# Performance work log

Hardware: AMD Instinct MI355X
Metric: run time of the kernel (lower is better)

## Reference

```python
import jax, jax.numpy as jnp
import numpy as np

HIDDEN = 128
N_RBF = 20
K = 16
CUTOFF = 5.0


def setup_inputs() -> dict:
    key = jax.random.key(0)
    ks = jax.random.split(key, 12)
    B, N, D = 8, 4096, HIDDEN
    edge_in = 2 * D + N_RBF  # 276
    s = 0.02
    return {
        "h": jax.random.normal(ks[0], (B, N, D), jnp.float32),
        "positions": jax.random.normal(ks[1], (B, N, 3), jnp.float32),
        # edge MLP: Linear(276->128), SiLU, Linear(128->128), SiLU
        "ew1": jax.random.normal(ks[2], (edge_in, D), jnp.float32) * s,
        "eb1": jnp.zeros((D,), jnp.float32),
        "ew2": jax.random.normal(ks[3], (D, D), jnp.float32) * s,
        "eb2": jnp.zeros((D,), jnp.float32),
        # node MLP: Linear(256->128), SiLU, (Dropout=identity in eval), Linear(128->128)
        "nw1": jax.random.normal(ks[4], (2 * D, D), jnp.float32) * s,
        "nb1": jnp.zeros((D,), jnp.float32),
        "nw2": jax.random.normal(ks[5], (D, D), jnp.float32) * s,
        "nb2": jnp.zeros((D,), jnp.float32),
        # LayerNorm
        "gamma": jnp.ones((D,), jnp.float32),
        "beta": jnp.zeros((D,), jnp.float32),
    }


def reference(h, positions, ew1, eb1, ew2, eb2, nw1, nb1, nw2, nb2, gamma, beta):
    B, N, D = h.shape
    k = min(K, N - 1)

    # ---- kNN graph build (dense pairwise, self masked with +inf) ----
    diff = positions[:, :, None, :] - positions[:, None, :, :]      # [B,N,N,3]
    dists = jnp.sqrt(jnp.sum(diff * diff, axis=-1) + 1e-8)          # [B,N,N]
    eye = jnp.eye(N, dtype=bool)
    dists_masked = jnp.where(eye[None], jnp.inf, dists)
    _, edge_idx = jax.lax.top_k(-dists_masked, k)                   # [B,N,k] smallest dists
    edge_dist = jnp.take_along_axis(dists_masked, edge_idx, axis=-1)  # [B,N,k]
    edge_mask = edge_dist < CUTOFF                                  # [B,N,k]

    # ---- RBF distance encoding (non-trainable buffers) ----
    centers = jnp.linspace(0.0, CUTOFF, N_RBF)                      # [n_rbf]
    widths = (CUTOFF / N_RBF) ** (-2)
    rbf = jnp.exp(-widths * (edge_dist[..., None] - centers) ** 2)  # [B,N,k,n_rbf]

    # ---- gather neighbor features ----
    h_j = jax.vmap(lambda hb, ib: hb[ib])(h, edge_idx)              # [B,N,k,D]
    h_i = jnp.broadcast_to(h[:, :, None, :], h_j.shape)             # [B,N,k,D]
    edge_features = jnp.concatenate([h_i, h_j, rbf], axis=-1)       # [B,N,k,2D+n_rbf]

    # ---- edge MLP + mask + scatter-sum aggregate ----
    m = jax.nn.silu(edge_features @ ew1 + eb1)
    m = jax.nn.silu(m @ ew2 + eb2)
    m = m * edge_mask[..., None].astype(m.dtype)
    agg = jnp.sum(m, axis=2)                                        # [B,N,D]

    # ---- node MLP (dropout is identity at eval) + residual + LayerNorm ----
    node_in = jnp.concatenate([h, agg], axis=-1)                    # [B,N,2D]
    update = jax.nn.silu(node_in @ nw1 + nb1) @ nw2 + nb2
    x = h + update
    mu = jnp.mean(x, axis=-1, keepdims=True)
    var = jnp.mean((x - mu) ** 2, axis=-1, keepdims=True)
    return (x - mu) / jnp.sqrt(var + 1e-5) * gamma + beta
```

## Files before the change

### kernel.cpp

```cpp
#include <hip/hip_runtime.h>

#define HID 128
#define NRBF 20
#define KNN 16
#define NNODE 4096
#define NBATCH 8
#define CAP 112

typedef __attribute__((ext_vector_type(8))) short short8;
typedef __attribute__((ext_vector_type(4))) float f32x4;

__device__ __forceinline__ short f2bf(float x) {
  unsigned u = __builtin_bit_cast(unsigned, x);
  u = u + 0x7FFFu + ((u >> 16) & 1u);
  return (short)(u >> 16);
}
__device__ __forceinline__ float silu_f(float x) {
  return x * __builtin_amdgcn_rcpf(1.0f + __expf(-x));
}
__device__ __forceinline__ short8 cv8(const float* p) {
  f32x4 a = *(const f32x4*)p;
  f32x4 b = *(const f32x4*)(p + 4);
  short8 r;
  r[0]=f2bf(a[0]); r[1]=f2bf(a[1]); r[2]=f2bf(a[2]); r[3]=f2bf(a[3]);
  r[4]=f2bf(b[0]); r[5]=f2bf(b[1]); r[6]=f2bf(b[2]); r[7]=f2bf(b[3]);
  return r;
}

__global__ __launch_bounds__(256)
void hcvt_kernel(const float* __restrict__ h, short* __restrict__ hb)
{
  size_t i = ((size_t)blockIdx.x * 256 + threadIdx.x) * 8;
  *(short8*)(hb + i) = cv8(h + i);
}

__global__ __launch_bounds__(512)
void knn_kernel(const float* __restrict__ pos,
                int* __restrict__ eidx, float* __restrict__ edist)
{
  __shared__ float pX[NNODE], pY[NNODE], pZ[NNODE];
  __shared__ float d2b[8][4][CAP];
  __shared__ int   jb[8][4][CAP];
  __shared__ int   cntL[8][4];

  const int tid  = threadIdx.x;
  const int wv   = tid >> 6;
  const int lane = tid & 63;
  const int b    = blockIdx.x >> 7;
  const int grp  = blockIdx.x & 127;

  const float* pb = pos + (size_t)b * NNODE * 3;
  for (int idx = tid; idx < NNODE; idx += 512) {
    pX[idx] = pb[idx*3]; pY[idx] = pb[idx*3+1]; pZ[idx] = pb[idx*3+2];
  }
  __syncthreads();

  const int i0 = grp * 32 + wv * 4;
  float pix[4], piy[4], piz[4];
  #pragma unroll
  for (int n = 0; n < 4; ++n) { pix[n]=pX[i0+n]; piy[n]=pY[i0+n]; piz[n]=pZ[i0+n]; }

  float vmin[4] = {3.0e38f, 3.0e38f, 3.0e38f, 3.0e38f};
  #pragma unroll 4
  for (int t = 0; t < 64; ++t) {
    const int j = t * 64 + lane;
    const float x = pX[j], y = pY[j], z = pZ[j];
    #pragma unroll
    for (int n = 0; n < 4; ++n) {
      float dx = pix[n] - x, dy = piy[n] - y, dz = piz[n] - z;
      float d2 = fmaf(dz, dz, fmaf(dy, dy, dx * dx));
      vmin[n] = fminf(vmin[n], d2);
    }
  }

  float Tp[4];
  #pragma unroll
  for (int n = 0; n < 4; ++n) {
    float v = vmin[n];
    #pragma unroll
    for (int k = 2; k <= 64; k <<= 1) {
      #pragma unroll
      for (int jj = k >> 1; jj > 0; jj >>= 1) {
        float o = __shfl_xor(v, jj);
        const bool up   = ((lane & k) == 0);
        const bool lowl = ((lane & jj) == 0);
        float mn = fminf(v, o), mx = fmaxf(v, o);
        v = (up == lowl) ? mn : mx;
      }
    }
    float Tf = __shfl(v, 16);
    Tp[n] = Tf * (1.0f + 2.0e-6f) + 1.0e-35f;
  }

  if (lane < 4) cntL[wv][lane] = 0;
  #pragma unroll 2
  for (int t = 0; t < 64; ++t) {
    const int j = t * 64 + lane;
    const float x = pX[j], y = pY[j], z = pZ[j];
    #pragma unroll
    for (int n = 0; n < 4; ++n) {
      float dx = pix[n] - x, dy = piy[n] - y, dz = piz[n] - z;
      float d2 = fmaf(dz, dz, fmaf(dy, dy, dx * dx));
      if ((j != i0 + n) && (d2 <= Tp[n])) {
        int p = atomicAdd(&cntL[wv][n], 1);
        if (p < CAP) jb[wv][n][p] = j;
      }
    }
  }

  #pragma unroll 1
  for (int n = 0; n < 4; ++n) {
    int cnt = cntL[wv][n];
    if (cnt > CAP) cnt = CAP;
    for (int s = lane; s < cnt; s += 64) {
      int j = jb[wv][n][s];
      float dx = __fsub_rn(pix[n], pX[j]);
      float dy = __fsub_rn(piy[n], pY[j]);
      float dz = __fsub_rn(piz[n], pZ[j]);
      d2b[wv][n][s] = __fadd_rn(__fadd_rn(__fmul_rn(dx,dx), __fmul_rn(dy,dy)),
                                __fmul_rn(dz,dz));
    }
    for (int s = lane; s < cnt; s += 64) {
      float dm = d2b[wv][n][s]; int jm = jb[wv][n][s];
      int rank = 0;
      for (int c = 0; c < cnt; ++c) {
        float dc = d2b[wv][n][c]; int jc = jb[wv][n][c];
        if (dc < dm || (dc == dm && jc < jm)) ++rank;
      }
      if (rank < KNN) {
        size_t base = ((size_t)b * NNODE + i0 + n) * KNN;
        eidx[base + rank]  = b * NNODE + jm;
        edist[base + rank] = sqrtf(__fadd_rn(dm, 1e-8f));
      }
    }
  }
}

#define ENPW 16

template<bool HBF>
__global__ __launch_bounds__(512)
void edge_kernel(const float* __restrict__ h, const short* __restrict__ hb,
                 const int* __restrict__ eidx, const float* __restrict__ edist,
                 const float* __restrict__ ew1, const float* __restrict__ eb1,
                 const float* __restrict__ ew2, const float* __restrict__ eb2,
                 float* __restrict__ agg)
{
  __shared__ __attribute__((aligned(16))) short8 F1[9*8*64];
  __shared__ __attribute__((aligned(16))) short8 F2[4*8*64];
  __shared__ __attribute__((aligned(16))) short m1s[8][2048];

  const int tid = threadIdx.x;
  for (int f = tid; f < 9*8*64; f += 512) {
    int kc = f >> 9, rem = f & 511, nf = rem >> 6, ln = rem & 63;
    int kb = kc*32 + (ln >> 4)*8, col = nf*16 + (ln & 15);
    short8 v;
    #pragma unroll
    for (int e = 0; e < 8; ++e) {
      int k = kb + e;
      v[e] = (k < 276) ? f2bf(ew1[k*128 + col]) : (short)0;
    }
    F1[f] = v;
  }
  for (int f = tid; f < 4*8*64; f += 512) {
    int kc = f >> 9, rem = f & 511, nf = rem >> 6, ln = rem & 63;
    int kb = kc*32 + (ln >> 4)*8, col = nf*16 + (ln & 15);
    short8 v;
    #pragma unroll
    for (int e = 0; e < 8; ++e) v[e] = f2bf(ew2[(kb + e)*128 + col]);
    F2[f] = v;
  }
  __syncthreads();

  const int wv = tid >> 6, lane = tid & 63;
  const int lo = lane & 15, hi = lane >> 4;
  short* m1w = &m1s[wv][0];

  float b1v[8], b2v[8];
  #pragma unroll
  for (int nf = 0; nf < 8; ++nf) {
    b1v[nf] = eb1[nf*16 + lo];
    b2v[nf] = eb2[nf*16 + lo];
  }
  int wbase[4], xmask[4], rbase[4];
  #pragma unroll
  for (int q = 0; q < 4; ++q) {
    int row = hi*4 + q;
    wbase[q] = (row << 8) + (lo << 1);
    xmask[q] = (row & 7) << 4;
  }
  #pragma unroll
  for (int kc = 0; kc < 4; ++kc)
    rbase[kc] = ((lo << 8) + ((kc*32 + hi*8) << 1)) ^ ((lo & 7) << 4);

  const f32x4 zero4 = {0.f, 0.f, 0.f, 0.f};
  const int nbase = (blockIdx.x * 8 + wv) * ENPW;

  #pragma unroll 1
  for (int it = 0; it < ENPW/2; ++it) {
    const int nA = nbase + it*2, nB = nA + 1;
    int jgA = eidx[(size_t)nA*KNN + lo] & (NBATCH*NNODE - 1);
    int jgB = eidx[(size_t)nB*KNN + lo] & (NBATCH*NNODE - 1);
    const float deA = edist[(size_t)nA*KNN + lo];
    const float deB = edist[(size_t)nB*KNN + lo];

    short8 aIA[4], aJA[4], aIB[4], aJB[4];
    #pragma unroll
    for (int kc = 0; kc < 4; ++kc) {
      if constexpr (HBF) {
        aIA[kc] = *(const short8*)(hb + (size_t)nA*HID  + kc*32 + hi*8);
        aJA[kc] = *(const short8*)(hb + (size_t)jgA*HID + kc*32 + hi*8);
        aIB[kc] = *(const short8*)(hb + (size_t)nB*HID  + kc*32 + hi*8);
        aJB[kc] = *(const short8*)(hb + (size_t)jgB*HID + kc*32 + hi*8);
      } else {
        aIA[kc] = cv8(h + (size_t)nA*HID  + kc*32 + hi*8);
        aJA[kc] = cv8(h + (size_t)jgA*HID + kc*32 + hi*8);
        aIB[kc] = cv8(h + (size_t)nB*HID  + kc*32 + hi*8);
        aJB[kc] = cv8(h + (size_t)jgB*HID + kc*32 + hi*8);
      }
    }
    short8 aRA, aRB;
    #pragma unroll
    for (int e = 0; e < 8; ++e) {
      const int r = hi*8 + e;
      float vA = 0.f, vB = 0.f;
      if (r < NRBF) {
        const float cr = (float)(r * (5.0/19.0));
        float tA = __fsub_rn(deA, cr), tB = __fsub_rn(deB, cr);
        vA = __expf(-16.0f * __fmul_rn(tA, tA));
        vB = __expf(-16.0f * __fmul_rn(tB, tB));
      }
      aRA[e] = f2bf(vA); aRB[e] = f2bf(vB);
    }

    f32x4 acc1A[8], acc1B[8];
    #pragma unroll
    for (int nf = 0; nf < 8; ++nf) { acc1A[nf] = zero4; acc1B[nf] = zero4; }
    __builtin_amdgcn_s_setprio(1);
    #pragma unroll
    for (int kc = 0; kc < 9; ++kc) {
      short8 aA = (kc < 4) ? aIA[kc] : ((kc < 8) ? aJA[kc-4] : aRA);
      short8 aB = (kc < 4) ? aIB[kc] : ((kc < 8) ? aJB[kc-4] : aRB);
      #pragma unroll
      for (int nf = 0; nf < 8; ++nf) {
        short8 bf = F1[(kc*8 + nf)*64 + lane];
        acc1A[nf] = __builtin_amdgcn_mfma_f32_16x16x32_bf16(aA, bf, acc1A[nf], 0,0,0);
        acc1B[nf] = __builtin_amdgcn_mfma_f32_16x16x32_bf16(aB, bf, acc1B[nf], 0,0,0);
      }
    }
    __builtin_amdgcn_s_setprio(0);

    short8 a2A[4], a2B[4];
    #pragma unroll
    for (int nf = 0; nf < 8; ++nf) {
      #pragma unroll
      for (int q = 0; q < 4; ++q) {
        int off = (wbase[q] + (nf << 5)) ^ xmask[q];
        *(short*)((char*)m1w + off) = f2bf(silu_f(acc1A[nf][q] + b1v[nf]));
      }
    }
    #pragma unroll
    for (int kc = 0; kc < 4; ++kc)
      a2A[kc] = *(const short8*)((char*)m1w + rbase[kc]);
    #pragma unroll
    for (int nf = 0; nf < 8; ++nf) {
      #pragma unroll
      for (int q = 0; q < 4; ++q) {
        int off = (wbase[q] + (nf << 5)) ^ xmask[q];
        *(short*)((char*)m1w + off) = f2bf(silu_f(acc1B[nf][q] + b1v[nf]));
      }
    }
    #pragma unroll
    for (int kc = 0; kc < 4; ++kc)
      a2B[kc] = *(const short8*)((char*)m1w + rbase[kc]);

    f32x4 acc2A[8], acc2B[8];
    #pragma unroll
    for (int nf = 0; nf < 8; ++nf) { acc2A[nf] = zero4; acc2B[nf] = zero4; }
    __builtin_amdgcn_s_setprio(1);
    #pragma unroll
    for (int kc = 0; kc < 4; ++kc) {
      #pragma unroll
      for (int nf = 0; nf < 8; ++nf) {
        short8 bf = F2[(kc*8 + nf)*64 + lane];
        acc2A[nf] = __builtin_amdgcn_mfma_f32_16x16x32_bf16(a2A[kc], bf, acc2A[nf], 0,0,0);
        acc2B[nf] = __builtin_amdgcn_mfma_f32_16x16x32_bf16(a2B[kc], bf, acc2B[nf], 0,0,0);
      }
    }
    __builtin_amdgcn_s_setprio(0);

    float dqA[4], dqB[4];
    #pragma unroll
    for (int q = 0; q < 4; ++q) {
      dqA[q] = __shfl(deA, hi*4 + q);
      dqB[q] = __shfl(deB, hi*4 + q);
    }
    #pragma unroll
    for (int nf = 0; nf < 8; ++nf) {
      float sA = 0.f, sB = 0.f;
      #pragma unroll
      for (int q = 0; q < 4; ++q) {
        float mA = silu_f(acc2A[nf][q] + b2v[nf]);
        float mB = silu_f(acc2B[nf][q] + b2v[nf]);
        sA += (dqA[q] < 5.0f) ? mA : 0.f;
        sB += (dqB[q] < 5.0f) ? mB : 0.f;
      }
      sA += __shfl_xor(sA, 16); sA += __shfl_xor(sA, 32);
      sB += __shfl_xor(sB, 16); sB += __shfl_xor(sB, 32);
      if (hi == 0) {
        agg[(size_t)nA*HID + nf*16 + lo] = sA;
        agg[(size_t)nB*HID + nf*16 + lo] = sB;
      }
    }
  }
}

template<bool HBF>
__global__ __launch_bounds__(512)
void node_kernel(const float* __restrict__ h, const short* __restrict__ hb,
                 const float* agg,
                 const float* __restrict__ nw1, const float* __restrict__ nb1,
                 const float* __restrict__ nw2, const float* __restrict__ nb2,
                 const float* __restrict__ gam, const float* __restrict__ bet,
                 float* out)
{
  __shared__ __attribute__((aligned(16))) short8 G1[8*8*64];
  __shared__ __attribute__((aligned(16))) short8 G2[4*8*64];
  __shared__ __attribute__((aligned(16))) short m1s[8][2048];

  const int tid = threadIdx.x;
  for (int f = tid; f < 8*8*64; f += 512) {
    int kc = f >> 9, rem = f & 511, nf = rem >> 6, ln = rem & 63;
    int kb = kc*32 + (ln >> 4)*8, col = nf*16 + (ln & 15);
    short8 v;
    #pragma unroll
    for (int e = 0; e < 8; ++e) v[e] = f2bf(nw1[(kb + e)*128 + col]);
    G1[f] = v;
  }
  for (int f = tid; f < 4*8*64; f += 512) {
    int kc = f >> 9, rem = f & 511, nf = rem >> 6, ln = rem & 63;
    int kb = kc*32 + (ln >> 4)*8, col = nf*16 + (ln & 15);
    short8 v;
    #pragma unroll
    for (int e = 0; e < 8; ++e) v[e] = f2bf(nw2[(kb + e)*128 + col]);
    G2[f] = v;
  }
  __syncthreads();

  const int wv = tid >> 6, lane = tid & 63;
  const int lo = lane & 15, hi = lane >> 4;
  short* m1w = &m1s[wv][0];

  float b1v[8], b2v[8], gv[8], bv[8];
  #pragma unroll
  for (int nf = 0; nf < 8; ++nf) {
    b1v[nf] = nb1[nf*16 + lo];
    b2v[nf] = nb2[nf*16 + lo];
    gv[nf]  = gam[nf*16 + lo];
    bv[nf]  = bet[nf*16 + lo];
  }
  const f32x4 zero4 = {0.f, 0.f, 0.f, 0.f};

  const int row0 = (blockIdx.x * 8 + wv) * 16;

  const float* hrow = h   + (size_t)(row0 + lo) * HID;
  const float* arow = agg + (size_t)(row0 + lo) * HID;
  const short* hbrow = hb + (size_t)(row0 + lo) * HID;

  f32x4 acc1[8];
  #pragma unroll
  for (int nf = 0; nf < 8; ++nf) acc1[nf] = zero4;
  #pragma unroll
  for (int kc = 0; kc < 8; ++kc) {
    short8 a;
    if (kc < 4) {
      if constexpr (HBF) a = *(const short8*)(hbrow + kc*32 + hi*8);
      else               a = cv8(hrow + kc*32 + hi*8);
    } else {
      a = cv8(arow + (kc - 4)*32 + hi*8);
    }
    #pragma unroll
    for (int nf = 0; nf < 8; ++nf) {
      short8 bf = G1[(kc*8 + nf)*64 + lane];
      acc1[nf] = __builtin_amdgcn_mfma_f32_16x16x32_bf16(a, bf, acc1[nf], 0,0,0);
    }
  }

  #pragma unroll
  for (int nf = 0; nf < 8; ++nf) {
    #pragma unroll
    for (int q = 0; q < 4; ++q) {
      float s = silu_f(acc1[nf][q] + b1v[nf]);
      int row = hi*4 + q, col = nf*16 + lo;
      int byteoff = ((row << 8) + (col << 1)) ^ ((row & 7) << 4);
      *(short*)((char*)m1w + byteoff) = f2bf(s);
    }
  }

  f32x4 acc2[8];
  #pragma unroll
  for (int nf = 0; nf < 8; ++nf) acc2[nf] = zero4;
  #pragma unroll
  for (int kc = 0; kc < 4; ++kc) {
    int byteA = ((lo << 8) + ((kc*32 + hi*8) << 1)) ^ ((lo & 7) << 4);
    short8 a = *(const short8*)((char*)m1w + byteA);
    #pragma unroll
    for (int nf = 0; nf < 8; ++nf) {
      short8 bf = G2[(kc*8 + nf)*64 + lane];
      acc2[nf] = __builtin_amdgcn_mfma_f32_16x16x32_bf16(a, bf, acc2[nf], 0,0,0);
    }
  }

  float xv[4][8];
  #pragma unroll
  for (int nf = 0; nf < 8; ++nf) {
    #pragma unroll
    for (int q = 0; q < 4; ++q) {
      xv[q][nf] = acc2[nf][q] + b2v[nf]
                + h[(size_t)(row0 + hi*4 + q) * HID + nf*16 + lo];
    }
  }

  #pragma unroll
  for (int q = 0; q < 4; ++q) {
    float s = 0.0f;
    #pragma unroll
    for (int nf = 0; nf < 8; ++nf) s += xv[q][nf];
    s += __shfl_xor(s, 1); s += __shfl_xor(s, 2);
    s += __shfl_xor(s, 4); s += __shfl_xor(s, 8);
    float mu = s * 0.0078125f;
    float t = 0.0f;
    #pragma unroll
    for (int nf = 0; nf < 8; ++nf) { float d = xv[q][nf] - mu; t += d * d; }
    t += __shfl_xor(t, 1); t += __shfl_xor(t, 2);
    t += __shfl_xor(t, 4); t += __shfl_xor(t, 8);
    float inv = 1.0f / sqrtf(t * 0.0078125f + 1e-5f);
    #pragma unroll
    for (int nf = 0; nf < 8; ++nf) {
      float y = (xv[q][nf] - mu) * inv * gv[nf] + bv[nf];
      out[(size_t)(row0 + hi*4 + q) * HID + nf*16 + lo] = y;
    }
  }
}

extern "C" void kernel_launch(void* const* d_in, const int* in_sizes, int n_in,
                              void* d_out, int out_size, void* d_ws, size_t ws_size,
                              hipStream_t stream) {
  (void)in_sizes; (void)n_in; (void)out_size;
  const float* h   = (const float*)d_in[0];
  const float* pos = (const float*)d_in[1];
  const float* ew1 = (const float*)d_in[2];
  const float* eb1 = (const float*)d_in[3];
  const float* ew2 = (const float*)d_in[4];
  const float* eb2 = (const float*)d_in[5];
  const float* nw1 = (const float*)d_in[6];
  const float* nb1 = (const float*)d_in[7];
  const float* nw2 = (const float*)d_in[8];
  const float* nb2 = (const float*)d_in[9];
  const float* gam = (const float*)d_in[10];
  const float* bet = (const float*)d_in[11];

  const size_t base_need = (size_t)NBATCH * NNODE * KNN * 8;
  const size_t hbf_need  = base_need + (size_t)NBATCH * NNODE * HID * 2;
  if (ws_size < base_need) return;
  const bool use_hbf = (ws_size >= hbf_need);

  char* wsp = (char*)d_ws;
  int*   eidx  = (int*)wsp;
  float* edist = (float*)(wsp + (size_t)NBATCH * NNODE * KNN * 4);
  short* hb    = (short*)(wsp + base_need);
  float* agg   = (float*)d_out;

  if (use_hbf) {
    hcvt_kernel<<<dim3(2048), dim3(256), 0, stream>>>(h, hb);
  }
  knn_kernel<<<dim3(1024), dim3(512), 0, stream>>>(pos, eidx, edist);
  if (use_hbf) {
    edge_kernel<true ><<<dim3(256), dim3(512), 0, stream>>>(h, hb, eidx, edist,
                                                            ew1, eb1, ew2, eb2, agg);
    node_kernel<true ><<<dim3(256), dim3(512), 0, stream>>>(h, hb, agg, nw1, nb1,
                                                            nw2, nb2, gam, bet, (float*)d_out);
  } else {
    edge_kernel<false><<<dim3(256), dim3(512), 0, stream>>>(h, hb, eidx, edist,
                                                            ew1, eb1, ew2, eb2, agg);
    node_kernel<false><<<dim3(256), dim3(512), 0, stream>>>(h, hb, agg, nw1, nb1,
                                                            nw2, nb2, gam, bet, (float*)d_out);
  }
}
```

Measured before the change: 203.5 us.

## Double-buffer edge-kernel gathers and split kNN min reduction into two chains

The edge kernel now software-pipelines its work: the neighbour and self feature gathers for the next pair of nodes are issued into a second register set while the current pair runs its MFMA chain, so global-load latency is meant to hide behind compute. The kNN threshold scan also processes two candidate columns per iteration with separate min accumulators, which shortens the dependency chain. In exchange, register pressure in the edge kernel roughly doubles for the A-operand fragments. That raises the risk of spills or lower occupancy at 512 threads per block.

```diff
diff --git a/kernel.cpp b/kernel.cpp
--- a/kernel.cpp
+++ b/kernel.cpp
@@ -60,23 +60,26 @@
   #pragma unroll
   for (int n = 0; n < 4; ++n) { pix[n]=pX[i0+n]; piy[n]=pY[i0+n]; piz[n]=pZ[i0+n]; }
 
-  float vmin[4] = {3.0e38f, 3.0e38f, 3.0e38f, 3.0e38f};
+  float vmin0[4] = {3.0e38f, 3.0e38f, 3.0e38f, 3.0e38f};
+  float vmin1[4] = {3.0e38f, 3.0e38f, 3.0e38f, 3.0e38f};
   #pragma unroll 4
-  for (int t = 0; t < 64; ++t) {
-    const int j = t * 64 + lane;
-    const float x = pX[j], y = pY[j], z = pZ[j];
+  for (int t = 0; t < 64; t += 2) {
+    const int j0 = t*64 + lane, j1 = j0 + 64;
+    const float x0 = pX[j0], y0 = pY[j0], z0 = pZ[j0];
+    const float x1 = pX[j1], y1 = pY[j1], z1 = pZ[j1];
     #pragma unroll
     for (int n = 0; n < 4; ++n) {
-      float dx = pix[n] - x, dy = piy[n] - y, dz = piz[n] - z;
-      float d2 = fmaf(dz, dz, fmaf(dy, dy, dx * dx));
-      vmin[n] = fminf(vmin[n], d2);
+      float dx0 = pix[n]-x0, dy0 = piy[n]-y0, dz0 = piz[n]-z0;
+      vmin0[n] = fminf(vmin0[n], fmaf(dz0,dz0, fmaf(dy0,dy0, dx0*dx0)));
+      float dx1 = pix[n]-x1, dy1 = piy[n]-y1, dz1 = piz[n]-z1;
+      vmin1[n] = fminf(vmin1[n], fmaf(dz1,dz1, fmaf(dy1,dy1, dx1*dx1)));
     }
   }
 
   float Tp[4];
   #pragma unroll
   for (int n = 0; n < 4; ++n) {
-    float v = vmin[n];
+    float v = fminf(vmin0[n], vmin1[n]);
     #pragma unroll
     for (int k = 2; k <= 64; k <<= 1) {
       #pragma unroll
@@ -139,6 +142,128 @@
 #define ENPW 16
 
 template<bool HBF>
+__device__ __forceinline__ void load_pair(const float* __restrict__ h,
+                 const short* __restrict__ hb,
+                 const int* __restrict__ eidx, const float* __restrict__ edist,
+                 int nA, int nB, int lo, int hi,
+                 short8 (&aIA)[4], short8 (&aJA)[4],
+                 short8 (&aIB)[4], short8 (&aJB)[4],
+                 float& deA, float& deB)
+{
+  int jgA = eidx[(size_t)nA*KNN + lo] & (NBATCH*NNODE - 1);
+  int jgB = eidx[(size_t)nB*KNN + lo] & (NBATCH*NNODE - 1);
+  deA = edist[(size_t)nA*KNN + lo];
+  deB = edist[(size_t)nB*KNN + lo];
+  #pragma unroll
+  for (int kc = 0; kc < 4; ++kc) {
+    if constexpr (HBF) {
+      aIA[kc] = *(const short8*)(hb + (size_t)nA*HID  + kc*32 + hi*8);
+      aJA[kc] = *(const short8*)(hb + (size_t)jgA*HID + kc*32 + hi*8);
+      aIB[kc] = *(const short8*)(hb + (size_t)nB*HID  + kc*32 + hi*8);
+      aJB[kc] = *(const short8*)(hb + (size_t)jgB*HID + kc*32 + hi*8);
+    } else {
+      aIA[kc] = cv8(h + (size_t)nA*HID  + kc*32 + hi*8);
+      aJA[kc] = cv8(h + (size_t)jgA*HID + kc*32 + hi*8);
+      aIB[kc] = cv8(h + (size_t)nB*HID  + kc*32 + hi*8);
+      aJB[kc] = cv8(h + (size_t)jgB*HID + kc*32 + hi*8);
+    }
+  }
+}
+
+#define COMPUTE_PAIR(AIA, AJA, AIB, AJB, DEA, DEB, NA, NB)                      \
+  do {                                                                          \
+    short8 aRA, aRB;                                                            \
+    _Pragma("unroll")                                                           \
+    for (int e = 0; e < 8; ++e) {                                               \
+      const int r = hi*8 + e;                                                   \
+      float vA = 0.f, vB = 0.f;                                                 \
+      if (r < NRBF) {                                                           \
+        const float cr = (float)(r * (5.0/19.0));                               \
+        float tA = __fsub_rn(DEA, cr), tB = __fsub_rn(DEB, cr);                 \
+        vA = __expf(-16.0f * __fmul_rn(tA, tA));                                \
+        vB = __expf(-16.0f * __fmul_rn(tB, tB));                                \
+      }                                                                         \
+      aRA[e] = f2bf(vA); aRB[e] = f2bf(vB);                                     \
+    }                                                                           \
+    f32x4 acc1A[8], acc1B[8];                                                   \
+    _Pragma("unroll")                                                           \
+    for (int nf = 0; nf < 8; ++nf) { acc1A[nf] = zero4; acc1B[nf] = zero4; }    \
+    __builtin_amdgcn_s_setprio(1);                                              \
+    _Pragma("unroll")                                                           \
+    for (int kc = 0; kc < 9; ++kc) {                                            \
+      short8 aA = (kc < 4) ? AIA[kc] : ((kc < 8) ? AJA[kc-4] : aRA);            \
+      short8 aB = (kc < 4) ? AIB[kc] : ((kc < 8) ? AJB[kc-4] : aRB);            \
+      _Pragma("unroll")                                                         \
+      for (int nf = 0; nf < 8; ++nf) {                                          \
+        short8 bfv = F1[(kc*8 + nf)*64 + lane];                                 \
+        acc1A[nf] = __builtin_amdgcn_mfma_f32_16x16x32_bf16(aA, bfv, acc1A[nf], 0,0,0); \
+        acc1B[nf] = __builtin_amdgcn_mfma_f32_16x16x32_bf16(aB, bfv, acc1B[nf], 0,0,0); \
+      }                                                                         \
+    }                                                                           \
+    __builtin_amdgcn_s_setprio(0);                                              \
+    short8 a2A[4], a2B[4];                                                      \
+    _Pragma("unroll")                                                           \
+    for (int nf = 0; nf < 8; ++nf) {                                            \
+      _Pragma("unroll")                                                         \
+      for (int q = 0; q < 4; ++q) {                                             \
+        int off = (wbase[q] + (nf << 5)) ^ xmask[q];                            \
+        *(short*)((char*)m1w + off) = f2bf(silu_f(acc1A[nf][q] + b1v[nf]));     \
+      }                                                                         \
+    }                                                                           \
+    _Pragma("unroll")                                                           \
+    for (int kc = 0; kc < 4; ++kc)                                              \
+      a2A[kc] = *(const short8*)((char*)m1w + rbase[kc]);                       \
+    _Pragma("unroll")                                                           \
+    for (int nf = 0; nf < 8; ++nf) {                                            \
+      _Pragma("unroll")                                                         \
+      for (int q = 0; q < 4; ++q) {                                             \
+        int off = (wbase[q] + (nf << 5)) ^ xmask[q];                            \
+        *(short*)((char*)m1w + off) = f2bf(silu_f(acc1B[nf][q] + b1v[nf]));     \
+      }                                                                         \
+    }                                                                           \
+    _Pragma("unroll")                                                           \
+    for (int kc = 0; kc < 4; ++kc)                                              \
+      a2B[kc] = *(const short8*)((char*)m1w + rbase[kc]);                       \
+    f32x4 acc2A[8], acc2B[8];                                                   \
+    _Pragma("unroll")                                                           \
+    for (int nf = 0; nf < 8; ++nf) { acc2A[nf] = zero4; acc2B[nf] = zero4; }    \
+    __builtin_amdgcn_s_setprio(1);                                              \
+    _Pragma("unroll")                                                           \
+    for (int kc = 0; kc < 4; ++kc) {                                            \
+      _Pragma("unroll")                                                         \
+      for (int nf = 0; nf < 8; ++nf) {                                          \
+        short8 bfv = F2[(kc*8 + nf)*64 + lane];                                 \
+        acc2A[nf] = __builtin_amdgcn_mfma_f32_16x16x32_bf16(a2A[kc], bfv, acc2A[nf], 0,0,0); \
+        acc2B[nf] = __builtin_amdgcn_mfma_f32_16x16x32_bf16(a2B[kc], bfv, acc2B[nf], 0,0,0); \
+      }                                                                         \
+    }                                                                           \
+    __builtin_amdgcn_s_setprio(0);                                              \
+    float dqA[4], dqB[4];                                                       \
+    _Pragma("unroll")                                                           \
+    for (int q = 0; q < 4; ++q) {                                               \
+      dqA[q] = __shfl(DEA, hi*4 + q);                                           \
+      dqB[q] = __shfl(DEB, hi*4 + q);                                           \
+    }                                                                           \
+    _Pragma("unroll")                                                           \
+    for (int nf = 0; nf < 8; ++nf) {                                            \
+      float sA = 0.f, sB = 0.f;                                                 \
+      _Pragma("unroll")                                                         \
+      for (int q = 0; q < 4; ++q) {                                             \
+        float mA = silu_f(acc2A[nf][q] + b2v[nf]);                              \
+        float mB = silu_f(acc2B[nf][q] + b2v[nf]);                              \
+        sA += (dqA[q] < 5.0f) ? mA : 0.f;                                       \
+        sB += (dqB[q] < 5.0f) ? mB : 0.f;                                       \
+      }                                                                         \
+      sA += __shfl_xor(sA, 16); sA += __shfl_xor(sA, 32);                       \
+      sB += __shfl_xor(sB, 16); sB += __shfl_xor(sB, 32);                       \
+      if (hi == 0) {                                                            \
+        agg[(size_t)(NA)*HID + nf*16 + lo] = sA;                                \
+        agg[(size_t)(NB)*HID + nf*16 + lo] = sB;                                \
+      }                                                                         \
+    }                                                                           \
+  } while (0)
+
+template<bool HBF>
 __global__ __launch_bounds__(512)
 void edge_kernel(const float* __restrict__ h, const short* __restrict__ hb,
                  const int* __restrict__ eidx, const float* __restrict__ edist,
@@ -196,122 +321,22 @@
   const f32x4 zero4 = {0.f, 0.f, 0.f, 0.f};
   const int nbase = (blockIdx.x * 8 + wv) * ENPW;
 
+  short8 p0IA[4], p0JA[4], p0IB[4], p0JB[4]; float p0dA, p0dB;
+  short8 p1IA[4], p1JA[4], p1IB[4], p1JB[4]; float p1dA, p1dB;
+
+  load_pair<HBF>(h, hb, eidx, edist, nbase+0, nbase+1, lo, hi,
+                 p0IA, p0JA, p0IB, p0JB, p0dA, p0dB);
+
   #pragma unroll 1
-  for (int it = 0; it < ENPW/2; ++it) {
-    const int nA = nbase + it*2, nB = nA + 1;
-    int jgA = eidx[(size_t)nA*KNN + lo] & (NBATCH*NNODE - 1);
-    int jgB = eidx[(size_t)nB*KNN + lo] & (NBATCH*NNODE - 1);
-    const float deA = edist[(size_t)nA*KNN + lo];
-    const float deB = edist[(size_t)nB*KNN + lo];
-
-    short8 aIA[4], aJA[4], aIB[4], aJB[4];
-    #pragma unroll
-    for (int kc = 0; kc < 4; ++kc) {
-      if constexpr (HBF) {
-        aIA[kc] = *(const short8*)(hb + (size_t)nA*HID  + kc*32 + hi*8);
-        aJA[kc] = *(const short8*)(hb + (size_t)jgA*HID + kc*32 + hi*8);
-        aIB[kc] = *(const short8*)(hb + (size_t)nB*HID  + kc*32 + hi*8);
-        aJB[kc] = *(const short8*)(hb + (size_t)jgB*HID + kc*32 + hi*8);
-      } else {
-        aIA[kc] = cv8(h + (size_t)nA*HID  + kc*32 + hi*8);
-        aJA[kc] = cv8(h + (size_t)jgA*HID + kc*32 + hi*8);
-        aIB[kc] = cv8(h + (size_t)nB*HID  + kc*32 + hi*8);
-        aJB[kc] = cv8(h + (size_t)jgB*HID + kc*32 + hi*8);
-      }
-    }
-    short8 aRA, aRB;
-    #pragma unroll
-    for (int e = 0; e < 8; ++e) {
-      const int r = hi*8 + e;
-      float vA = 0.f, vB = 0.f;
-      if (r < NRBF) {
-        const float cr = (float)(r * (5.0/19.0));
-        float tA = __fsub_rn(deA, cr), tB = __fsub_rn(deB, cr);
-        vA = __expf(-16.0f * __fmul_rn(tA, tA));
-        vB = __expf(-16.0f * __fmul_rn(tB, tB));
-      }
-      aRA[e] = f2bf(vA); aRB[e] = f2bf(vB);
-    }
-
-    f32x4 acc1A[8], acc1B[8];
-    #pragma unroll
-    for (int nf = 0; nf < 8; ++nf) { acc1A[nf] = zero4; acc1B[nf] = zero4; }
-    __builtin_amdgcn_s_setprio(1);
-    #pragma unroll
-    for (int kc = 0; kc < 9; ++kc) {
-      short8 aA = (kc < 4) ? aIA[kc] : ((kc < 8) ? aJA[kc-4] : aRA);
-      short8 aB = (kc < 4) ? aIB[kc] : ((kc < 8) ? aJB[kc-4] : aRB);
-      #pragma unroll
-      for (int nf = 0; nf < 8; ++nf) {
-        short8 bf = F1[(kc*8 + nf)*64 + lane];
-        acc1A[nf] = __builtin_amdgcn_mfma_f32_16x16x32_bf16(aA, bf, acc1A[nf], 0,0,0);
-        acc1B[nf] = __builtin_amdgcn_mfma_f32_16x16x32_bf16(aB, bf, acc1B[nf], 0,0,0);
-      }
-    }
-    __builtin_amdgcn_s_setprio(0);
-
-    short8 a2A[4], a2B[4];
-    #pragma unroll
-    for (int nf = 0; nf < 8; ++nf) {
-      #pragma unroll
-      for (int q = 0; q < 4; ++q) {
-        int off = (wbase[q] + (nf << 5)) ^ xmask[q];
-        *(short*)((char*)m1w + off) = f2bf(silu_f(acc1A[nf][q] + b1v[nf]));
-      }
-    }
-    #pragma unroll
-    for (int kc = 0; kc < 4; ++kc)
-      a2A[kc] = *(const short8*)((char*)m1w + rbase[kc]);
-    #pragma unroll
-    for (int nf = 0; nf < 8; ++nf) {
-      #pragma unroll
-      for (int q = 0; q < 4; ++q) {
-        int off = (wbase[q] + (nf << 5)) ^ xmask[q];
-        *(short*)((char*)m1w + off) = f2bf(silu_f(acc1B[nf][q] + b1v[nf]));
-      }
-    }
-    #pragma unroll
-    for (int kc = 0; kc < 4; ++kc)
-      a2B[kc] = *(const short8*)((char*)m1w + rbase[kc]);
-
-    f32x4 acc2A[8], acc2B[8];
-    #pragma unroll
-    for (int nf = 0; nf < 8; ++nf) { acc2A[nf] = zero4; acc2B[nf] = zero4; }
-    __builtin_amdgcn_s_setprio(1);
-    #pragma unroll
-    for (int kc = 0; kc < 4; ++kc) {
-      #pragma unroll
-      for (int nf = 0; nf < 8; ++nf) {
-        short8 bf = F2[(kc*8 + nf)*64 + lane];
-        acc2A[nf] = __builtin_amdgcn_mfma_f32_16x16x32_bf16(a2A[kc], bf, acc2A[nf], 0,0,0);
-        acc2B[nf] = __builtin_amdgcn_mfma_f32_16x16x32_bf16(a2B[kc], bf, acc2B[nf], 0,0,0);
-      }
-    }
-    __builtin_amdgcn_s_setprio(0);
-
-    float dqA[4], dqB[4];
-    #pragma unroll
-    for (int q = 0; q < 4; ++q) {
-      dqA[q] = __shfl(deA, hi*4 + q);
-      dqB[q] = __shfl(deB, hi*4 + q);
-    }
-    #pragma unroll
-    for (int nf = 0; nf < 8; ++nf) {
-      float sA = 0.f, sB = 0.f;
-      #pragma unroll
-      for (int q = 0; q < 4; ++q) {
-        float mA = silu_f(acc2A[nf][q] + b2v[nf]);
-        float mB = silu_f(acc2B[nf][q] + b2v[nf]);
-        sA += (dqA[q] < 5.0f) ? mA : 0.f;
-        sB += (dqB[q] < 5.0f) ? mB : 0.f;
-      }
-      sA += __shfl_xor(sA, 16); sA += __shfl_xor(sA, 32);
-      sB += __shfl_xor(sB, 16); sB += __shfl_xor(sB, 32);
-      if (hi == 0) {
-        agg[(size_t)nA*HID + nf*16 + lo] = sA;
-        agg[(size_t)nB*HID + nf*16 + lo] = sB;
-      }
-    }
+  for (int it2 = 0; it2 < 4; ++it2) {
+    const int base = nbase + it2*4;
+    load_pair<HBF>(h, hb, eidx, edist, base+2, base+3, lo, hi,
+                   p1IA, p1JA, p1IB, p1JB, p1dA, p1dB);
+    COMPUTE_PAIR(p0IA, p0JA, p0IB, p0JB, p0dA, p0dB, base, base+1);
+    if (it2 < 3)
+      load_pair<HBF>(h, hb, eidx, edist, base+4, base+5, lo, hi,
+                     p0IA, p0JA, p0IB, p0JB, p0dA, p0dB);
+    COMPUTE_PAIR(p1IA, p1JA, p1IB, p1JB, p1dA, p1dB, base+2, base+3);
   }
 }
 
@@ -381,8 +406,8 @@
     }
     #pragma unroll
     for (int nf = 0; nf < 8; ++nf) {
-      short8 bf = G1[(kc*8 + nf)*64 + lane];
-      acc1[nf] = __builtin_amdgcn_mfma_f32_16x16x32_bf16(a, bf, acc1[nf], 0,0,0);
+      short8 bfv = G1[(kc*8 + nf)*64 + lane];
+      acc1[nf] = __builtin_amdgcn_mfma_f32_16x16x32_bf16(a, bfv, acc1[nf], 0,0,0);
     }
   }
 
@@ -406,8 +431,8 @@
     short8 a = *(const short8*)((char*)m1w + byteA);
     #pragma unroll
     for (int nf = 0; nf < 8; ++nf) {
-      short8 bf = G2[(kc*8 + nf)*64 + lane];
-      acc2[nf] = __builtin_amdgcn_mfma_f32_16x16x32_bf16(a, bf, acc2[nf], 0,0,0);
+      short8 bfv = G2[(kc*8 + nf)*64 + lane];
+      acc2[nf] = __builtin_amdgcn_mfma_f32_16x16x32_bf16(a, bfv, acc2[nf], 0,0,0);
     }
   }
 
```

Measured after the change: 248.5 us. 1.22x slower.
